# Optimization experiments

Hardware: AMD Instinct MI355X
Metric: run time of the kernel (lower is better)

## Reference

```python
import jax, jax.numpy as jnp
import numpy as np

N_X, DIS, IN, OUT = 40000, 10000, 128, 64
N = N_X + DIS
E = 800000
BN_EPS = 1e-5


def setup_inputs() -> dict:
    key = jax.random.key(0)
    ks = jax.random.split(key, 20)

    def glorot(k, shape):
        fan_in, fan_out = shape[-2], shape[-1]
        a = np.sqrt(6.0 / (fan_in + fan_out)).astype(np.float32)
        return jax.random.uniform(k, shape, jnp.float32, -a, a)

    return {
        "x": jax.random.normal(ks[0], (N_X, IN), jnp.float32),
        "emb": jax.random.uniform(ks[1], (DIS, IN), jnp.float32),
        "conv1_w": glorot(ks[2], (3, IN, 2 * OUT)),
        "conv1_root": glorot(ks[3], (IN, 2 * OUT)),
        "conv1_bias": jnp.zeros((2 * OUT,), jnp.float32),
        "conv2_w": glorot(ks[4], (3, 2 * OUT, 4 * OUT)),
        "conv2_root": glorot(ks[5], (2 * OUT, 4 * OUT)),
        "conv2_bias": jnp.zeros((4 * OUT,), jnp.float32),
        "convinf_w": glorot(ks[6], (3, 4 * OUT, 4 * OUT)),
        "convinf_root": glorot(ks[7], (4 * OUT, 4 * OUT)),
        "convinf_bias": jnp.zeros((4 * OUT,), jnp.float32),
        "conv3_w": glorot(ks[8], (3, 4 * OUT, OUT)),
        "conv3_root": glorot(ks[9], (4 * OUT, OUT)),
        "conv3_bias": jnp.zeros((OUT,), jnp.float32),
        "norm1_g": jnp.ones((2 * OUT,), jnp.float32),
        "norm1_b": jnp.zeros((2 * OUT,), jnp.float32),
        "norm2_g": jnp.ones((4 * OUT,), jnp.float32),
        "norm2_b": jnp.zeros((4 * OUT,), jnp.float32),
        "edge_index": jax.random.randint(ks[10], (2, E), 0, N),
        "edge_types": jax.random.randint(ks[11], (E,), 0, 3),
    }


def reference(x, emb, conv1_w, conv1_root, conv1_bias, conv2_w, conv2_root,
              conv2_bias, convinf_w, convinf_root, convinf_bias, conv3_w,
              conv3_root, conv3_bias, norm1_g, norm1_b, norm2_g, norm2_b,
              edge_index, edge_types):
    dst, src = edge_index[0], edge_index[1]  # adj_t row = target, col = source
    n = x.shape[0] + emb.shape[0]

    # gcn_norm without self-loops: deg over rows, w_e = d^-1/2[dst] * d^-1/2[src]
    deg = jax.ops.segment_sum(jnp.ones(dst.shape[0], jnp.float32), dst, num_segments=n)
    dis = jnp.where(deg > 0, jax.lax.rsqrt(jnp.maximum(deg, 1.0)), 0.0)
    ew = dis[dst] * dis[src]  # [E]

    def wrgcn(h, W, root, bias):
        out = h @ root + bias
        h_src = h[src]  # [E, d] gather (dominant memory traffic)
        for r in range(3):
            w_r = jnp.where(edge_types == r, ew, 0.0)
            agg = jax.ops.segment_sum(w_r[:, None] * h_src, dst, num_segments=n)
            out = out + agg @ W[r]
        return out

    def bn(h, g, b):
        m = h.mean(axis=0)
        v = jnp.var(h, axis=0)  # biased, matches torch BN training normalization
        return (h - m) * jax.lax.rsqrt(v + BN_EPS) * g + b

    h0 = jnp.concatenate([x, emb], axis=0)  # [N, IN]
    x1 = bn(wrgcn(h0, conv1_w, conv1_root, conv1_bias), norm1_g, norm1_b)
    x2 = bn(wrgcn(jax.nn.relu(x1), conv2_w, conv2_root, conv2_bias), norm2_g, norm2_b)
    for _ in range(5):
        x2 = bn(wrgcn(jax.nn.relu(x2), convinf_w, convinf_root, convinf_bias), norm2_g, norm2_b)
    return wrgcn(jax.nn.relu(x2), conv3_w, conv3_root, conv3_bias)
```

## Files before the change

kernel.cpp:

```cpp
#include <hip/hip_runtime.h>

#define N_X  40000
#define NN   50000
#define NE   800000
#define MPAD 50048

using short8  = __attribute__((ext_vector_type(8))) short;
using floatx4 = __attribute__((ext_vector_type(4))) float;
using uintx2  = __attribute__((ext_vector_type(2))) unsigned int;
using uintx4  = __attribute__((ext_vector_type(4))) unsigned int;

typedef const __attribute__((address_space(1))) void gv_t;
typedef __attribute__((address_space(3))) void lv_t;

__device__ __forceinline__ unsigned short f2bf(float f) {
  unsigned u = __float_as_uint(f);
  u += 0x7FFF + ((u >> 16) & 1);
  return (unsigned short)(u >> 16);
}
__device__ __forceinline__ float bf2f(unsigned v) {
  return __uint_as_float(v << 16);
}
__device__ __forceinline__ float h2f(unsigned v) {
  unsigned short s = (unsigned short)v;
  _Float16 f;
  __builtin_memcpy(&f, &s, 2);
  return (float)f;
}
__device__ __forceinline__ unsigned short f2h(float f) {
  _Float16 h = (_Float16)f;
  unsigned short s;
  __builtin_memcpy(&s, &h, 2);
  return s;
}

__global__ void k_deg(const int* __restrict__ dst, int* __restrict__ deg) {
  int e = blockIdx.x * blockDim.x + threadIdx.x;
  if (e < NE) atomicAdd(&deg[dst[e]], 1);
}

__global__ void k_dis(const int* __restrict__ deg, float* __restrict__ dis) {
  int i = blockIdx.x * blockDim.x + threadIdx.x;
  if (i < NN) dis[i] = deg[i] > 0 ? rsqrtf((float)deg[i]) : 0.f;
}

#define SCAN_B 1024
#define SCAN_NB 49
__global__ void k_scan1(const int* __restrict__ deg, int* __restrict__ rowp,
                        int* __restrict__ bsum) {
  __shared__ int buf[SCAN_B];
  int b = blockIdx.x;
  int i = b * SCAN_B + threadIdx.x;
  int v = (i < NN) ? deg[i] : 0;
  buf[threadIdx.x] = v;
  __syncthreads();
  for (int off = 1; off < SCAN_B; off <<= 1) {
    int t = (threadIdx.x >= off) ? buf[threadIdx.x - off] : 0;
    __syncthreads();
    buf[threadIdx.x] += t;
    __syncthreads();
  }
  if (i < NN) rowp[i] = buf[threadIdx.x] - v;
  if (threadIdx.x == SCAN_B - 1) bsum[b] = buf[SCAN_B - 1];
}

__global__ void k_scan2(int* __restrict__ bsum) {
  if (threadIdx.x == 0) {
    int acc = 0;
    for (int i = 0; i < SCAN_NB; ++i) { int t = bsum[i]; bsum[i] = acc; acc += t; }
  }
}

__global__ void k_scan3(int* __restrict__ rowp, const int* __restrict__ bsum) {
  int i = blockIdx.x * blockDim.x + threadIdx.x;
  if (i < NN) rowp[i] += bsum[i >> 10];
  if (i == 0) rowp[NN] = NE;
}

__global__ void k_build(const int* __restrict__ dst, const int* __restrict__ src,
                        const int* __restrict__ typ, const float* __restrict__ dis,
                        const int* __restrict__ rowp, int* __restrict__ cur,
                        uintx2* __restrict__ ed) {
  int e = blockIdx.x * blockDim.x + threadIdx.x;
  if (e >= NE) return;
  int d = dst[e], s = src[e];
  int p = rowp[d] + atomicAdd(&cur[d], 1);
  uintx2 v;
  v.x = (unsigned)s | ((unsigned)typ[e] << 28);
  v.y = __float_as_uint(dis[d] * dis[s]);
  ed[p] = v;
}

__global__ void k_prep0(const float* __restrict__ x, const float* __restrict__ emb,
                        unsigned short* __restrict__ Gh, unsigned short* __restrict__ Gl) {
  int idx = blockIdx.x * blockDim.x + threadIdx.x;
  if (idx >= NN * 32) return;
  int r = idx >> 5;
  const float* srcp = (r < N_X) ? (x + (size_t)idx * 4)
                                : (emb + ((size_t)idx - (size_t)N_X * 32) * 4);
  float4 hv = *(const float4*)srcp;
  float vv[4] = {hv.x, hv.y, hv.z, hv.w};
  unsigned hw[2], lw[2];
#pragma unroll
  for (int q = 0; q < 2; ++q) {
    unsigned short h0 = f2bf(vv[2 * q]), h1 = f2bf(vv[2 * q + 1]);
    unsigned short l0 = f2bf(vv[2 * q] - bf2f(h0)), l1 = f2bf(vv[2 * q + 1] - bf2f(h1));
    hw[q] = (unsigned)h0 | ((unsigned)h1 << 16);
    lw[q] = (unsigned)l0 | ((unsigned)l1 << 16);
  }
  size_t o = (size_t)idx * 4;
  *(uintx2*)(Gh + o) = uintx2{hw[0], hw[1]};
  *(uintx2*)(Gl + o) = uintx2{lw[0], lw[1]};
}

__global__ void k_prep(const float* __restrict__ H, const float* __restrict__ sc,
                       const float* __restrict__ sh, unsigned short* __restrict__ Gh,
                       unsigned short* __restrict__ Gl, int din) {
  int idx = blockIdx.x * blockDim.x + threadIdx.x;
  if (idx >= NN * (din >> 2)) return;
  int c4 = (idx & ((din >> 2) - 1)) * 4;
  float4 hv = *(const float4*)(H + (size_t)idx * 4);
  float vv[4] = {hv.x, hv.y, hv.z, hv.w};
#pragma unroll
  for (int q = 0; q < 4; ++q)
    vv[q] = fmaxf(vv[q] * sc[c4 + q] + sh[c4 + q], 0.f);
  unsigned hw[2], lw[2];
#pragma unroll
  for (int q = 0; q < 2; ++q) {
    unsigned short h0 = f2bf(vv[2 * q]), h1 = f2bf(vv[2 * q + 1]);
    unsigned short l0 = f2bf(vv[2 * q] - bf2f(h0)), l1 = f2bf(vv[2 * q + 1] - bf2f(h1));
    hw[q] = (unsigned)h0 | ((unsigned)h1 << 16);
    lw[q] = (unsigned)l0 | ((unsigned)l1 << 16);
  }
  size_t o = (size_t)idx * 4;
  *(uintx2*)(Gh + o) = uintx2{hw[0], hw[1]};
  *(uintx2*)(Gl + o) = uintx2{lw[0], lw[1]};
}

__global__ void k_wcat2(const float* __restrict__ root, const float* __restrict__ W,
                        unsigned short* __restrict__ BhT, unsigned short* __restrict__ BlT,
                        int din, int dout) {
  int idx = blockIdx.x * blockDim.x + threadIdx.x;
  if (idx >= 4 * dout * din) return;
  int n = idx / din, k = idx % din;
  float v;
  if (n < dout) v = root[(size_t)k * dout + n];
  else {
    int r = n / dout - 1, c = n % dout;
    v = W[((size_t)r * din + k) * dout + c];
  }
  unsigned short h = f2bf(v);
  BhT[idx] = h;
  BlT[idx] = f2bf(v - bf2f(h));
}

__global__ __launch_bounds__(256, 3) void k_gemm2(
    const unsigned short* __restrict__ Ah, const unsigned short* __restrict__ Al,
    const unsigned short* __restrict__ Bh, const unsigned short* __restrict__ Bl,
    float* __restrict__ Rroot, unsigned short* __restrict__ P,
    int M, int K, int dout, int ny) {
  constexpr int TC = 24;
  constexpr int CPW = 6;
  constexpr int NT = 2;
  __shared__ __align__(16) char lds[2][TC * 1024];

  const int tid = threadIdx.x;
  const int lane = tid & 63;
  const int w = tid >> 6;
  const int wm = w >> 1, wn = w & 1;
  const int r16 = lane & 15, kg = lane >> 4;

  const int nwg = gridDim.x;
  const int q = nwg >> 3, r = nwg & 7;
  const int xcd = blockIdx.x & 7, pos = blockIdx.x >> 3;
  const int t = (xcd < r ? xcd * (q + 1) : r * (q + 1) + (xcd - r) * q) + pos;
  const int bm = (t / ny) * 128;
  const int bn = (t % ny) * 64;

  const int rowseg = lane >> 2;
  const int seg = (lane & 3) ^ ((lane >> 3) & 3);
  const unsigned short* gb[CPW];
#pragma unroll
  for (int i = 0; i < CPW; ++i) {
    int c = w * CPW + i;
    const unsigned short* base;
    int row0;
    if (c < 16) { base = (c < 8) ? Ah : Al; row0 = bm + (c & 7) * 16; }
    else        { int cc = c - 16; base = (cc < 4) ? Bh : Bl; row0 = bn + (cc & 3) * 16; }
    gb[i] = base + (size_t)(row0 + rowseg) * K + seg * 8;
  }

  floatx4 acc[4][NT];
#pragma unroll
  for (int i = 0; i < 4; ++i)
#pragma unroll
    for (int jj = 0; jj < NT; ++jj) acc[i][jj] = (floatx4)0.f;

  const int nk = K >> 5;

  auto stage = [&](int b, int tk) {
#pragma unroll
    for (int i = 0; i < CPW; ++i)
      __builtin_amdgcn_global_load_lds((gv_t*)(gb[i] + tk * 32),
                                       (lv_t*)&lds[b][(w * CPW + i) * 1024],
                                       16, 0, 0);
  };

  stage(0, 0);
  stage(1, 1);

  const int fo = r16 * 64 + ((kg ^ ((r16 >> 1) & 3)) * 16);

  int buf = 0;
  for (int tk = 0; tk < nk; ++tk) {
    if (tk < nk - 1) asm volatile("s_waitcnt vmcnt(6)" ::: "memory");
    else             asm volatile("s_waitcnt vmcnt(0)" ::: "memory");
    __builtin_amdgcn_s_barrier();

    const char* Lb = lds[buf];
    short8 ah[4], al[4], bh[NT], bl[NT];
#pragma unroll
    for (int mt = 0; mt < 4; ++mt) {
      ah[mt] = *(const short8*)(Lb + (wm * 4 + mt) * 1024 + fo);
      al[mt] = *(const short8*)(Lb + (8 + wm * 4 + mt) * 1024 + fo);
    }
#pragma unroll
    for (int nt = 0; nt < NT; ++nt) {
      bh[nt] = *(const short8*)(Lb + (16 + wn * NT + nt) * 1024 + fo);
      bl[nt] = *(const short8*)(Lb + (20 + wn * NT + nt) * 1024 + fo);
    }

    __builtin_amdgcn_s_setprio(1);
#pragma unroll
    for (int mt = 0; mt < 4; ++mt)
#pragma unroll
      for (int nt = 0; nt < NT; ++nt) {
        acc[mt][nt] = __builtin_amdgcn_mfma_f32_16x16x32_bf16(ah[mt], bh[nt], acc[mt][nt], 0, 0, 0);
        acc[mt][nt] = __builtin_amdgcn_mfma_f32_16x16x32_bf16(ah[mt], bl[nt], acc[mt][nt], 0, 0, 0);
        acc[mt][nt] = __builtin_amdgcn_mfma_f32_16x16x32_bf16(al[mt], bh[nt], acc[mt][nt], 0, 0, 0);
      }
    __builtin_amdgcn_s_setprio(0);

    __builtin_amdgcn_s_barrier();
    if (tk + 2 < nk) stage(buf, tk + 2);
    buf ^= 1;
  }

  const int sec = bn / dout;
  const int cb = bn - sec * dout;
#pragma unroll
  for (int mt = 0; mt < 4; ++mt) {
    const int gr0 = bm + wm * 64 + mt * 16 + kg * 4;
#pragma unroll
    for (int nt = 0; nt < NT; ++nt) {
      const int colL = cb + wn * 32 + nt * 16 + r16;
#pragma unroll
      for (int rr = 0; rr < 4; ++rr) {
        const int gr = gr0 + rr;
        if (gr >= M) continue;
        const float o = acc[mt][nt][rr];
        if (sec == 0) Rroot[(size_t)gr * dout + colL] = o;
        else          P[((size_t)gr * 3 + (sec - 1)) * dout + colL] = f2h(o);
      }
    }
  }
}

template <int L>
__global__ void k_agg2(const unsigned short* __restrict__ P,
                       const float* __restrict__ Rroot,
                       const float* __restrict__ bias,
                       const int* __restrict__ rowp, const uintx2* __restrict__ ed,
                       float* __restrict__ Out, int dout) {
  constexpr int G = 64 / L;
  const int wid = (blockIdx.x * 256 + threadIdx.x) >> 6;
  if (wid >= NN) return;
  const int lane = threadIdx.x & 63;
  const int grp = lane / L;
  const int c0 = (lane & (L - 1)) * 4;
  const int beg = rowp[wid], end = rowp[wid + 1];
  float a[4] = {};
  for (int i = beg + grp; i < end; i += G) {
    const uintx2 e = ed[i];
    const float wv = __uint_as_float(e.y);
    const unsigned tt = e.x >> 28;
    const size_t off = ((size_t)(e.x & 0x0FFFFFFFu) * 3 + tt) * dout + c0;
    const uintx2 g = *(const uintx2*)(P + off);
    a[0] += wv * h2f(g.x & 0xFFFFu);
    a[1] += wv * h2f(g.x >> 16);
    a[2] += wv * h2f(g.y & 0xFFFFu);
    a[3] += wv * h2f(g.y >> 16);
  }
  if constexpr (G > 1) {
#pragma unroll
    for (int off = L; off < 64; off <<= 1) {
#pragma unroll
      for (int qq = 0; qq < 4; ++qq) a[qq] += __shfl_xor(a[qq], off);
    }
  }
  if (grp == 0) {
    const float4 bv = *(const float4*)(bias + c0);
    const float4 rv = *(const float4*)(Rroot + (size_t)wid * dout + c0);
    float4 o;
    o.x = rv.x + bv.x + a[0];
    o.y = rv.y + bv.y + a[1];
    o.z = rv.z + bv.z + a[2];
    o.w = rv.w + bv.w + a[3];
    *(float4*)(Out + (size_t)wid * dout + c0) = o;
  }
}

__global__ void k_bnstats(const float* __restrict__ H, float* __restrict__ sums, int d) {
  int c = threadIdx.x;
  float s = 0.f, s2 = 0.f;
  for (int r = blockIdx.x; r < NN; r += gridDim.x) {
    float v = H[(size_t)r * d + c];
    s += v;
    s2 += v * v;
  }
  atomicAdd(&sums[c], s);
  atomicAdd(&sums[d + c], s2);
}

__global__ void k_bnfinal(const float* __restrict__ sums, const float* __restrict__ g,
                          const float* __restrict__ b, float* __restrict__ sc,
                          float* __restrict__ sh, int d) {
  int c = threadIdx.x;
  if (c >= d) return;
  float mean = sums[c] * (1.f / NN);
  float var = sums[d + c] * (1.f / NN) - mean * mean;
  float rs = rsqrtf(var + 1e-5f);
  float s = rs * g[c];
  sc[c] = s;
  sh[c] = b[c] - mean * s;
}

extern "C" void kernel_launch(void* const* d_in, const int* in_sizes, int n_in,
                              void* d_out, int out_size, void* d_ws, size_t ws_size,
                              hipStream_t stream) {
  const float* x   = (const float*)d_in[0];
  const float* emb = (const float*)d_in[1];
  const float* conv_w[4] = {(const float*)d_in[2], (const float*)d_in[5],
                            (const float*)d_in[8], (const float*)d_in[11]};
  const float* conv_r[4] = {(const float*)d_in[3], (const float*)d_in[6],
                            (const float*)d_in[9], (const float*)d_in[12]};
  const float* conv_b[4] = {(const float*)d_in[4], (const float*)d_in[7],
                            (const float*)d_in[10], (const float*)d_in[13]};
  const float* n1g = (const float*)d_in[14];
  const float* n1b = (const float*)d_in[15];
  const float* n2g = (const float*)d_in[16];
  const float* n2b = (const float*)d_in[17];
  const int* eidx = (const int*)d_in[18];
  const int* etyp = (const int*)d_in[19];
  const int* dst  = eidx;
  const int* srcp = eidx + NE;
  float* out = (float*)d_out;

  char* w = (char*)d_ws;
  auto alloc = [&](size_t bytes) {
    char* p = w;
    w += (bytes + 255) & ~(size_t)255;
    return p;
  };
  unsigned short* Gh   = (unsigned short*)alloc((size_t)MPAD * 256 * 2);
  unsigned short* Gl   = (unsigned short*)alloc((size_t)MPAD * 256 * 2);
  unsigned short* P    = (unsigned short*)alloc((size_t)MPAD * 768 * 2);
  float*    Rroot = (float*)alloc((size_t)MPAD * 256 * 4);
  float*    H    = (float*)alloc((size_t)NN * 256 * 4);
  unsigned short* WcTh = (unsigned short*)alloc((size_t)1024 * 256 * 2);
  unsigned short* WcTl = (unsigned short*)alloc((size_t)1024 * 256 * 2);
  float*    bns  = (float*)alloc(512 * 4);
  float*    bsc  = (float*)alloc(256 * 4);
  float*    bsh  = (float*)alloc(256 * 4);
  float*    dis  = (float*)alloc((size_t)NN * 4);
  int*      deg  = (int*)alloc((size_t)NN * 4);
  int*      rowp = (int*)alloc((size_t)(NN + 1) * 4);
  int*      cur  = (int*)alloc((size_t)NN * 4);
  int*      bsum = (int*)alloc(64 * 4);
  uintx2*   ed   = (uintx2*)alloc((size_t)NE * 8);

  hipMemsetAsync(deg, 0, (size_t)NN * 4, stream);
  hipMemsetAsync(cur, 0, (size_t)NN * 4, stream);
  k_deg<<<(NE + 255) / 256, 256, 0, stream>>>(dst, deg);
  k_dis<<<(NN + 255) / 256, 256, 0, stream>>>(deg, dis);
  k_scan1<<<SCAN_NB, SCAN_B, 0, stream>>>(deg, rowp, bsum);
  k_scan2<<<1, 64, 0, stream>>>(bsum);
  k_scan3<<<(NN + 255) / 256, 256, 0, stream>>>(rowp, bsum);
  k_build<<<(NE + 255) / 256, 256, 0, stream>>>(dst, srcp, etyp, dis, rowp, cur, ed);

  const int din_a[8]  = {128, 128, 256, 256, 256, 256, 256, 256};
  const int dout_a[8] = {128, 256, 256, 256, 256, 256, 256, 64};
  const int wi_a[8]   = {0, 1, 2, 2, 2, 2, 2, 3};
  const int gm = (NN + 127) / 128;

  for (int l = 0; l < 8; ++l) {
    const int din = din_a[l], dout = dout_a[l];
    const int wi = wi_a[l];

    if (l == 0)
      k_prep0<<<(NN * 32 + 255) / 256, 256, 0, stream>>>(x, emb, Gh, Gl);
    else
      k_prep<<<(NN * (din >> 2) + 255) / 256, 256, 0, stream>>>(H, bsc, bsh, Gh, Gl, din);

    k_wcat2<<<(4 * dout * din + 255) / 256, 256, 0, stream>>>(conv_r[wi], conv_w[wi],
                                                              WcTh, WcTl, din, dout);

    const int ny = 4 * dout / 64;
    k_gemm2<<<gm * ny, 256, 0, stream>>>(Gh, Gl, WcTh, WcTl, Rroot, P, NN, din, dout, ny);

    float* O = (l == 7) ? out : H;
    if (dout == 256)
      k_agg2<64><<<(NN + 3) / 4, 256, 0, stream>>>(P, Rroot, conv_b[wi], rowp, ed, O, dout);
    else if (dout == 128)
      k_agg2<32><<<(NN + 3) / 4, 256, 0, stream>>>(P, Rroot, conv_b[wi], rowp, ed, O, dout);
    else
      k_agg2<16><<<(NN + 3) / 4, 256, 0, stream>>>(P, Rroot, conv_b[wi], rowp, ed, O, dout);

    if (l < 7) {
      hipMemsetAsync(bns, 0, (size_t)2 * dout * 4, stream);
      k_bnstats<<<256, dout, 0, stream>>>(H, bns, dout);
      k_bnfinal<<<1, 256, 0, stream>>>(bns, (l == 0) ? n1g : n2g,
                                       (l == 0) ? n1b : n2b, bsc, bsh, dout);
    }
  }
}
```

Baseline: 1.859 ms.

## Enlarge GEMM M-tile, widen aggregation loads, hoist weight conversion out of layer loop

The GEMM tile doubles to 256 rows per workgroup, with eight M-subtiles per wave and the occupancy hint lowered to 2, so each B fragment load is reused more. The aggregation kernel now makes 16-byte gathers of 8 fp16 values per lane, so fewer lanes cover a row and more edge groups run in parallel. Weight concatenation and bf16 splitting now run once per distinct weight before the layer loop instead of once per layer. The costs are more LDS and register pressure, lower occupancy, and extra padding work on the last M tile.

```diff
diff --git a/kernel.cpp b/kernel.cpp
--- a/kernel.cpp
+++ b/kernel.cpp
@@ -154,13 +154,13 @@
   BlT[idx] = f2bf(v - bf2f(h));
 }
 
-__global__ __launch_bounds__(256, 3) void k_gemm2(
+__global__ __launch_bounds__(256, 2) void k_gemm2(
     const unsigned short* __restrict__ Ah, const unsigned short* __restrict__ Al,
     const unsigned short* __restrict__ Bh, const unsigned short* __restrict__ Bl,
     float* __restrict__ Rroot, unsigned short* __restrict__ P,
     int M, int K, int dout, int ny) {
-  constexpr int TC = 24;
-  constexpr int CPW = 6;
+  constexpr int TC = 40;
+  constexpr int CPW = 10;
   constexpr int NT = 2;
   __shared__ __align__(16) char lds[2][TC * 1024];
 
@@ -174,7 +174,7 @@
   const int q = nwg >> 3, r = nwg & 7;
   const int xcd = blockIdx.x & 7, pos = blockIdx.x >> 3;
   const int t = (xcd < r ? xcd * (q + 1) : r * (q + 1) + (xcd - r) * q) + pos;
-  const int bm = (t / ny) * 128;
+  const int bm = (t / ny) * 256;
   const int bn = (t % ny) * 64;
 
   const int rowseg = lane >> 2;
@@ -185,14 +185,16 @@
     int c = w * CPW + i;
     const unsigned short* base;
     int row0;
-    if (c < 16) { base = (c < 8) ? Ah : Al; row0 = bm + (c & 7) * 16; }
-    else        { int cc = c - 16; base = (cc < 4) ? Bh : Bl; row0 = bn + (cc & 3) * 16; }
+    if (c < 16)      { base = Ah; row0 = bm + c * 16; }
+    else if (c < 32) { base = Al; row0 = bm + (c - 16) * 16; }
+    else if (c < 36) { base = Bh; row0 = bn + (c - 32) * 16; }
+    else             { base = Bl; row0 = bn + (c - 36) * 16; }
     gb[i] = base + (size_t)(row0 + rowseg) * K + seg * 8;
   }
 
-  floatx4 acc[4][NT];
-#pragma unroll
-  for (int i = 0; i < 4; ++i)
+  floatx4 acc[8][NT];
+#pragma unroll
+  for (int i = 0; i < 8; ++i)
 #pragma unroll
     for (int jj = 0; jj < NT; ++jj) acc[i][jj] = (floatx4)0.f;
 
@@ -213,32 +215,30 @@
 
   int buf = 0;
   for (int tk = 0; tk < nk; ++tk) {
-    if (tk < nk - 1) asm volatile("s_waitcnt vmcnt(6)" ::: "memory");
+    if (tk < nk - 1) asm volatile("s_waitcnt vmcnt(10)" ::: "memory");
     else             asm volatile("s_waitcnt vmcnt(0)" ::: "memory");
     __builtin_amdgcn_s_barrier();
 
     const char* Lb = lds[buf];
-    short8 ah[4], al[4], bh[NT], bl[NT];
-#pragma unroll
-    for (int mt = 0; mt < 4; ++mt) {
-      ah[mt] = *(const short8*)(Lb + (wm * 4 + mt) * 1024 + fo);
-      al[mt] = *(const short8*)(Lb + (8 + wm * 4 + mt) * 1024 + fo);
+    short8 bh[NT], bl[NT];
+#pragma unroll
+    for (int nt = 0; nt < NT; ++nt) {
+      bh[nt] = *(const short8*)(Lb + (32 + wn * NT + nt) * 1024 + fo);
+      bl[nt] = *(const short8*)(Lb + (36 + wn * NT + nt) * 1024 + fo);
     }
-#pragma unroll
-    for (int nt = 0; nt < NT; ++nt) {
-      bh[nt] = *(const short8*)(Lb + (16 + wn * NT + nt) * 1024 + fo);
-      bl[nt] = *(const short8*)(Lb + (20 + wn * NT + nt) * 1024 + fo);
+
+    __builtin_amdgcn_s_setprio(1);
+#pragma unroll
+    for (int mt = 0; mt < 8; ++mt) {
+      short8 ah = *(const short8*)(Lb + (wm * 8 + mt) * 1024 + fo);
+      short8 al = *(const short8*)(Lb + (16 + wm * 8 + mt) * 1024 + fo);
+#pragma unroll
+      for (int nt = 0; nt < NT; ++nt) {
+        acc[mt][nt] = __builtin_amdgcn_mfma_f32_16x16x32_bf16(ah, bh[nt], acc[mt][nt], 0, 0, 0);
+        acc[mt][nt] = __builtin_amdgcn_mfma_f32_16x16x32_bf16(ah, bl[nt], acc[mt][nt], 0, 0, 0);
+        acc[mt][nt] = __builtin_amdgcn_mfma_f32_16x16x32_bf16(al, bh[nt], acc[mt][nt], 0, 0, 0);
+      }
     }
-
-    __builtin_amdgcn_s_setprio(1);
-#pragma unroll
-    for (int mt = 0; mt < 4; ++mt)
-#pragma unroll
-      for (int nt = 0; nt < NT; ++nt) {
-        acc[mt][nt] = __builtin_amdgcn_mfma_f32_16x16x32_bf16(ah[mt], bh[nt], acc[mt][nt], 0, 0, 0);
-        acc[mt][nt] = __builtin_amdgcn_mfma_f32_16x16x32_bf16(ah[mt], bl[nt], acc[mt][nt], 0, 0, 0);
-        acc[mt][nt] = __builtin_amdgcn_mfma_f32_16x16x32_bf16(al[mt], bh[nt], acc[mt][nt], 0, 0, 0);
-      }
     __builtin_amdgcn_s_setprio(0);
 
     __builtin_amdgcn_s_barrier();
@@ -249,8 +249,8 @@
   const int sec = bn / dout;
   const int cb = bn - sec * dout;
 #pragma unroll
-  for (int mt = 0; mt < 4; ++mt) {
-    const int gr0 = bm + wm * 64 + mt * 16 + kg * 4;
+  for (int mt = 0; mt < 8; ++mt) {
+    const int gr0 = bm + wm * 128 + mt * 16 + kg * 4;
 #pragma unroll
     for (int nt = 0; nt < NT; ++nt) {
       const int colL = cb + wn * 32 + nt * 16 + r16;
@@ -271,42 +271,53 @@
                        const float* __restrict__ Rroot,
                        const float* __restrict__ bias,
                        const int* __restrict__ rowp, const uintx2* __restrict__ ed,
-                       float* __restrict__ Out, int dout) {
+                       float* __restrict__ Out) {
   constexpr int G = 64 / L;
+  constexpr int dout = L * 8;
   const int wid = (blockIdx.x * 256 + threadIdx.x) >> 6;
   if (wid >= NN) return;
   const int lane = threadIdx.x & 63;
   const int grp = lane / L;
-  const int c0 = (lane & (L - 1)) * 4;
+  const int c0 = (lane & (L - 1)) * 8;
   const int beg = rowp[wid], end = rowp[wid + 1];
-  float a[4] = {};
+  float a[8] = {};
   for (int i = beg + grp; i < end; i += G) {
     const uintx2 e = ed[i];
     const float wv = __uint_as_float(e.y);
     const unsigned tt = e.x >> 28;
     const size_t off = ((size_t)(e.x & 0x0FFFFFFFu) * 3 + tt) * dout + c0;
-    const uintx2 g = *(const uintx2*)(P + off);
+    const uintx4 g = *(const uintx4*)(P + off);
     a[0] += wv * h2f(g.x & 0xFFFFu);
     a[1] += wv * h2f(g.x >> 16);
     a[2] += wv * h2f(g.y & 0xFFFFu);
     a[3] += wv * h2f(g.y >> 16);
-  }
-  if constexpr (G > 1) {
-#pragma unroll
-    for (int off = L; off < 64; off <<= 1) {
-#pragma unroll
-      for (int qq = 0; qq < 4; ++qq) a[qq] += __shfl_xor(a[qq], off);
-    }
+    a[4] += wv * h2f(g.z & 0xFFFFu);
+    a[5] += wv * h2f(g.z >> 16);
+    a[6] += wv * h2f(g.w & 0xFFFFu);
+    a[7] += wv * h2f(g.w >> 16);
+  }
+#pragma unroll
+  for (int off = L; off < 64; off <<= 1) {
+#pragma unroll
+    for (int qq = 0; qq < 8; ++qq) a[qq] += __shfl_xor(a[qq], off);
   }
   if (grp == 0) {
-    const float4 bv = *(const float4*)(bias + c0);
-    const float4 rv = *(const float4*)(Rroot + (size_t)wid * dout + c0);
-    float4 o;
-    o.x = rv.x + bv.x + a[0];
-    o.y = rv.y + bv.y + a[1];
-    o.z = rv.z + bv.z + a[2];
-    o.w = rv.w + bv.w + a[3];
-    *(float4*)(Out + (size_t)wid * dout + c0) = o;
+    const size_t ob = (size_t)wid * dout + c0;
+    const float4 bv0 = *(const float4*)(bias + c0);
+    const float4 bv1 = *(const float4*)(bias + c0 + 4);
+    const float4 rv0 = *(const float4*)(Rroot + ob);
+    const float4 rv1 = *(const float4*)(Rroot + ob + 4);
+    float4 o0, o1;
+    o0.x = rv0.x + bv0.x + a[0];
+    o0.y = rv0.y + bv0.y + a[1];
+    o0.z = rv0.z + bv0.z + a[2];
+    o0.w = rv0.w + bv0.w + a[3];
+    o1.x = rv1.x + bv1.x + a[4];
+    o1.y = rv1.y + bv1.y + a[5];
+    o1.z = rv1.z + bv1.z + a[6];
+    o1.w = rv1.w + bv1.w + a[7];
+    *(float4*)(Out + ob) = o0;
+    *(float4*)(Out + ob + 4) = o1;
   }
 }
 
@@ -367,8 +378,12 @@
   unsigned short* P    = (unsigned short*)alloc((size_t)MPAD * 768 * 2);
   float*    Rroot = (float*)alloc((size_t)MPAD * 256 * 4);
   float*    H    = (float*)alloc((size_t)NN * 256 * 4);
-  unsigned short* WcTh = (unsigned short*)alloc((size_t)1024 * 256 * 2);
-  unsigned short* WcTl = (unsigned short*)alloc((size_t)1024 * 256 * 2);
+  unsigned short* WTh[4];
+  unsigned short* WTl[4];
+  for (int i = 0; i < 4; ++i) {
+    WTh[i] = (unsigned short*)alloc((size_t)1024 * 256 * 2);
+    WTl[i] = (unsigned short*)alloc((size_t)1024 * 256 * 2);
+  }
   float*    bns  = (float*)alloc(512 * 4);
   float*    bsc  = (float*)alloc(256 * 4);
   float*    bsh  = (float*)alloc(256 * 4);
@@ -391,7 +406,13 @@
   const int din_a[8]  = {128, 128, 256, 256, 256, 256, 256, 256};
   const int dout_a[8] = {128, 256, 256, 256, 256, 256, 256, 64};
   const int wi_a[8]   = {0, 1, 2, 2, 2, 2, 2, 3};
-  const int gm = (NN + 127) / 128;
+  const int gm = (MPAD + 255) / 256;
+
+  const int wdin[4]  = {128, 128, 256, 256};
+  const int wdout[4] = {128, 256, 256, 64};
+  for (int i = 0; i < 4; ++i)
+    k_wcat2<<<(4 * wdout[i] * wdin[i] + 255) / 256, 256, 0, stream>>>(
+        conv_r[i], conv_w[i], WTh[i], WTl[i], wdin[i], wdout[i]);
 
   for (int l = 0; l < 8; ++l) {
     const int din = din_a[l], dout = dout_a[l];
@@ -402,19 +423,16 @@
     else
       k_prep<<<(NN * (din >> 2) + 255) / 256, 256, 0, stream>>>(H, bsc, bsh, Gh, Gl, din);
 
-    k_wcat2<<<(4 * dout * din + 255) / 256, 256, 0, stream>>>(conv_r[wi], conv_w[wi],
-                                                              WcTh, WcTl, din, dout);
-
     const int ny = 4 * dout / 64;
-    k_gemm2<<<gm * ny, 256, 0, stream>>>(Gh, Gl, WcTh, WcTl, Rroot, P, NN, din, dout, ny);
+    k_gemm2<<<gm * ny, 256, 0, stream>>>(Gh, Gl, WTh[wi], WTl[wi], Rroot, P, NN, din, dout, ny);
 
     float* O = (l == 7) ? out : H;
     if (dout == 256)
-      k_agg2<64><<<(NN + 3) / 4, 256, 0, stream>>>(P, Rroot, conv_b[wi], rowp, ed, O, dout);
+      k_agg2<32><<<(NN + 3) / 4, 256, 0, stream>>>(P, Rroot, conv_b[wi], rowp, ed, O);
     else if (dout == 128)
-      k_agg2<32><<<(NN + 3) / 4, 256, 0, stream>>>(P, Rroot, conv_b[wi], rowp, ed, O, dout);
+      k_agg2<16><<<(NN + 3) / 4, 256, 0, stream>>>(P, Rroot, conv_b[wi], rowp, ed, O);
     else
-      k_agg2<16><<<(NN + 3) / 4, 256, 0, stream>>>(P, Rroot, conv_b[wi], rowp, ed, O, dout);
+      k_agg2<8><<<(NN + 3) / 4, 256, 0, stream>>>(P, Rroot, conv_b[wi], rowp, ed, O);
 
     if (l < 7) {
       hipMemsetAsync(bns, 0, (size_t)2 * dout * 4, stream);
```

Measured after the change: 1.757 ms. 5.5% less time.
